# Optimization experiments

Hardware: AMD Instinct MI355X
Metric: run time of the kernel (lower is better)

## Reference

```python
import jax, jax.numpy as jnp
import numpy as np

B = 1 << 21          # shading points per batch
U_RES, CH = 400, 8   # spatial plane
A_RES, ACH = 50, 50 and 8  # placeholder, real consts below
A_RES, ACH = 50, 8   # angular planes (h/d)
HID = 32
IN_CH = CH + 2 * ACH  # 24


def _bilerp_clamp(tex, uv):
    # Bilinear interp, both axes clamped (U-plane). tex: (H,W,C), uv: (B,2) in [0,1]
    H, W, _ = tex.shape
    u = jnp.clip(uv[:, 0], 0.0, 1.0) * (W - 1)
    v = jnp.clip(uv[:, 1], 0.0, 1.0) * (H - 1)
    x0 = jnp.floor(u).astype(jnp.int32)
    x1 = jnp.clip(x0 + 1, 0, W - 1)
    y0 = jnp.floor(v).astype(jnp.int32)
    y1 = jnp.clip(y0 + 1, 0, H - 1)
    ur = (u - x0.astype(u.dtype))[:, None]
    vr = (v - y0.astype(v.dtype))[:, None]
    p00 = tex[y0, x0]; p10 = tex[y0, x1]; p01 = tex[y1, x0]; p11 = tex[y1, x1]
    return ((1 - ur) * (1 - vr) * p00 + ur * (1 - vr) * p10
            + (1 - ur) * vr * p01 + ur * vr * p11)


def _bilerp_wrap_u(tex, uv):
    # Bilinear interp wrapping the u (phi) axis, clamping v (H/D planes).
    H, W, _ = tex.shape
    u = (uv[:, 0] % 1.0) * W
    v = jnp.clip(uv[:, 1], 0.0, 1.0) * (H - 1)
    x0f = jnp.floor(u)
    x0 = x0f.astype(jnp.int32) % W
    x1 = (x0 + 1) % W
    y0 = jnp.floor(v).astype(jnp.int32)
    y1 = jnp.clip(y0 + 1, 0, H - 1)
    ur = (u - x0f)[:, None]
    vr = (v - y0.astype(v.dtype))[:, None]
    p00 = tex[y0, x0]; p10 = tex[y0, x1]; p01 = tex[y1, x0]; p11 = tex[y1, x1]
    return ((1 - ur) * (1 - vr) * p00 + ur * (1 - vr) * p10
            + (1 - ur) * vr * p01 + ur * vr * p11)


def setup_inputs() -> dict:
    key = jax.random.key(0)
    ks = jax.random.split(key, 8)
    x = jax.random.uniform(ks[0], (B, 6), dtype=jnp.float32)
    u_plane = 0.01 * jax.random.normal(ks[1], (U_RES, U_RES, CH), dtype=jnp.float32)
    h_plane = 0.01 * jax.random.normal(ks[2], (A_RES, A_RES, ACH), dtype=jnp.float32)
    d_plane = 0.01 * jax.random.normal(ks[3], (A_RES, A_RES, ACH), dtype=jnp.float32)
    def lin_w(k, fout, fin):  # torch nn.Linear default init (kaiming-uniform-ish)
        lim = 1.0 / np.sqrt(fin)
        return jax.random.uniform(k, (fout, fin), jnp.float32, -lim, lim)
    W0 = lin_w(ks[4], HID, IN_CH)
    W1 = lin_w(ks[5], HID, HID)
    W2 = lin_w(ks[6], HID, HID)
    W3 = lin_w(ks[7], 3, HID)
    return {"x": x, "u_plane": u_plane, "h_plane": h_plane, "d_plane": d_plane,
            "W0": W0, "W1": W1, "W2": W2, "W3": W3}


def reference(x, u_plane, h_plane, d_plane, W0, W1, W2, W3):
    # Split and reorder: H/D planes receive (u=phi, v=theta)
    uv = x[:, 0:2]
    h_uv = jnp.stack((x[:, 3], x[:, 2]), axis=1)
    d_uv = jnp.stack((x[:, 5], x[:, 4]), axis=1)
    fU = _bilerp_clamp(u_plane, uv)       # (B, CH)
    fH = _bilerp_wrap_u(h_plane, h_uv)    # (B, ACH)
    fD = _bilerp_wrap_u(d_plane, d_uv)    # (B, ACH)
    feat = jnp.concatenate([fU, fH, fD], axis=1)  # (B, 24)
    # Quant mode 'off' -> QLinear is a plain bias-free matmul with W^T
    h = jax.nn.relu(feat @ W0.T)
    h = jax.nn.relu(h @ W1.T)
    h = jax.nn.relu(h @ W2.T)
    return h @ W3.T  # (B, 3)
```

## Files before the change

kernel.cpp:

```cpp
#include <hip/hip_runtime.h>

typedef _Float16 half4 __attribute__((ext_vector_type(4)));
typedef _Float16 half8 __attribute__((ext_vector_type(8)));
typedef float floatx4 __attribute__((ext_vector_type(4)));

#define U_RESV 400
#define A_RESV 50

#define UHALVES (U_RESV * U_RESV * 8)
#define AHALVES (A_RESV * A_RESV * 8)
#define WOFF    (UHALVES + 2 * AHALVES)
#define W0OFF   0
#define W1OFF   896
#define W2OFF   2048
#define W3OFF   3200
#define WTOT    3776

__device__ __forceinline__ float clamp01(float x) { return fminf(fmaxf(x, 0.0f), 1.0f); }

__device__ __forceinline__ floatx4 mfma16(half4 a, half4 b, floatx4 c) {
    return __builtin_amdgcn_mfma_f32_16x16x16f16(a, b, c, 0, 0, 0);
}
__device__ __forceinline__ half4 zero4() {
    half4 h; h[0] = h[1] = h[2] = h[3] = (_Float16)0.f; return h;
}
__device__ __forceinline__ half4 relu4(half4 v) {
#if __has_builtin(__builtin_elementwise_max)
    return __builtin_elementwise_max(v, zero4());
#else
    half4 r;
#pragma unroll
    for (int i = 0; i < 4; ++i) r[i] = v[i] > (_Float16)0.f ? v[i] : (_Float16)0.f;
    return r;
#endif
}

__device__ __forceinline__ void cvt_chunk(const float* __restrict__ src,
                                          _Float16* __restrict__ dst, int i) {
    float4 a = *(const float4*)(src + (size_t)i * 8);
    float4 b = *(const float4*)(src + (size_t)i * 8 + 4);
    half8 h;
    h[0] = (_Float16)a.x; h[1] = (_Float16)a.y; h[2] = (_Float16)a.z; h[3] = (_Float16)a.w;
    h[4] = (_Float16)b.x; h[5] = (_Float16)b.y; h[6] = (_Float16)b.z; h[7] = (_Float16)b.w;
    *(half8*)(dst + (size_t)i * 8) = h;
}

__device__ __forceinline__ void wblob_fill(const float* __restrict__ W0,
                                           const float* __restrict__ W1,
                                           const float* __restrict__ W2,
                                           const float* __restrict__ W3,
                                           _Float16* __restrict__ w, int tid, int nthr) {
    for (int i = tid; i < WTOT; i += nthr) {
        float v;
        if (i < W1OFF) {
            int r = i / 28, c = i - r * 28;
            v = (c < 24) ? W0[r * 24 + c] : 0.f;
        } else if (i < W2OFF) {
            int j = i - W1OFF, r = j / 36, c = j - r * 36;
            v = (c < 32) ? W1[r * 32 + c] : 0.f;
        } else if (i < W3OFF) {
            int j = i - W2OFF, r = j / 36, c = j - r * 36;
            v = (c < 32) ? W2[r * 32 + c] : 0.f;
        } else {
            int j = i - W3OFF, r = j / 36, c = j - r * 36;
            v = (r < 3 && c < 32) ? W3[r * 32 + c] : 0.f;
        }
        w[i] = (_Float16)v;
    }
}

__global__ __launch_bounds__(256) void pconv_kernel(
    const float* __restrict__ u_plane, const float* __restrict__ h_plane,
    const float* __restrict__ d_plane, const float* __restrict__ W0,
    const float* __restrict__ W1, const float* __restrict__ W2,
    const float* __restrict__ W3, _Float16* __restrict__ dst) {
    const int gid = blockIdx.x * 256 + threadIdx.x;
    const int gsz = gridDim.x * 256;
    for (int i = gid; i < UHALVES / 8; i += gsz) cvt_chunk(u_plane, dst, i);
    for (int i = gid; i < AHALVES / 8; i += gsz) cvt_chunk(h_plane, dst + UHALVES, i);
    for (int i = gid; i < AHALVES / 8; i += gsz) cvt_chunk(d_plane, dst + UHALVES + AHALVES, i);
    if (blockIdx.x == 0) wblob_fill(W0, W1, W2, W3, dst + WOFF, threadIdx.x, 256);
}

__global__ __launch_bounds__(256) void wprep_kernel(
    const float* __restrict__ W0, const float* __restrict__ W1,
    const float* __restrict__ W2, const float* __restrict__ W3,
    _Float16* __restrict__ wdst) {
    wblob_fill(W0, W1, W2, W3, wdst, threadIdx.x, 256);
}

struct GA { int o0, o1, o2, o3; float w00, w10, w01, w11; };

__device__ __forceinline__ GA mkU(float ux, float uy) {
    GA g;
    float u = clamp01(ux) * (float)(U_RESV - 1);
    float v = clamp01(uy) * (float)(U_RESV - 1);
    float x0f = floorf(u), y0f = floorf(v);
    int x0 = (int)x0f, y0 = (int)y0f;
    int x1 = min(x0 + 1, U_RESV - 1), y1 = min(y0 + 1, U_RESV - 1);
    float ur = u - x0f, vr = v - y0f;
    g.w00 = (1.0f - ur) * (1.0f - vr); g.w10 = ur * (1.0f - vr);
    g.w01 = (1.0f - ur) * vr;          g.w11 = ur * vr;
    g.o0 = (y0 * U_RESV + x0) * 8;
    g.o1 = (y0 * U_RESV + x1) * 8;
    g.o2 = (y1 * U_RESV + x0) * 8;
    g.o3 = (y1 * U_RESV + x1) * 8;
    return g;
}
__device__ __forceinline__ GA mkA(float uu, float vv) {
    GA g;
    float uf = uu - floorf(uu);
    float u = uf * (float)A_RESV;
    float v = clamp01(vv) * (float)(A_RESV - 1);
    float x0f = floorf(u), y0f = floorf(v);
    int x0 = (int)x0f;
    int x1 = x0 + 1; if (x1 == A_RESV) x1 = 0;
    int y0 = (int)y0f;
    int y1 = min(y0 + 1, A_RESV - 1);
    float ur = u - x0f, vr = v - y0f;
    g.w00 = (1.0f - ur) * (1.0f - vr); g.w10 = ur * (1.0f - vr);
    g.w01 = (1.0f - ur) * vr;          g.w11 = ur * vr;
    g.o0 = (y0 * A_RESV + x0) * 8;
    g.o1 = (y0 * A_RESV + x1) * 8;
    g.o2 = (y1 * A_RESV + x0) * 8;
    g.o3 = (y1 * A_RESV + x1) * 8;
    return g;
}

__device__ __forceinline__ void blend8(half8 a, half8 b, half8 c, half8 d,
                                       const GA& g, float* f) {
#pragma unroll
    for (int i = 0; i < 8; ++i) {
        float r = (float)a[i] * g.w00;
        r = fmaf((float)b[i], g.w10, r);
        r = fmaf((float)c[i], g.w01, r);
        r = fmaf((float)d[i], g.w11, r);
        f[i] = r;
    }
}


template <int K>
__global__ __launch_bounds__(256, 2) void tpmlp_pipe(
    const float* __restrict__ x,
    const _Float16* __restrict__ up,
    const _Float16* __restrict__ hp,
    const _Float16* __restrict__ dp,
    const _Float16* __restrict__ wsw,
    float* __restrict__ out) {
    const int tid  = threadIdx.x;
    const int lane = tid & 63;
    const int wv   = tid >> 6;
    const int q    = lane >> 4;
    const int c15  = lane & 15;

    __shared__ __align__(16) _Float16 fl[256 * 28];
    __shared__ __align__(16) _Float16 wl[WTOT];

    {
        const uint4* src = (const uint4*)wsw;
        uint4 a = src[tid];
        uint4 b;
        if (tid < 472 - 256) b = src[256 + tid];
        uint4* dst = (uint4*)wl;
        dst[tid] = a;
        if (tid < 472 - 256) dst[256 + tid] = b;
    }
    __syncthreads();

    const _Float16* wb  = fl + (size_t)wv * 64 * 28;
    const _Float16* w0l = wl + W0OFF;
    const _Float16* w1l = wl + W1OFF;
    const _Float16* w2l = wl + W2OFF;
    const _Float16* w3l = wl + W3OFF;
    const size_t blkbase = (size_t)blockIdx.x * (256 * K);

    auto xload = [&](int it, float2& a, float2& b, float2& c) {
        const float2* p = (const float2*)(x + (blkbase + (size_t)it * 256 + tid) * 6);
        a = p[0]; b = p[1]; c = p[2];
    };

    float2 c01, c23, c45;
    float2 n01, n23, n45;
    xload(0, c01, c23, c45);
    if (K > 1) xload(1, n01, n23, n45);

    GA gU = mkU(c01.x, c01.y);
    GA gH = mkA(c23.y, c23.x);
    GA gD = mkA(c45.y, c45.x);
    half8 tU0 = *(const half8*)(up + gU.o0);
    half8 tU1 = *(const half8*)(up + gU.o1);
    half8 tU2 = *(const half8*)(up + gU.o2);
    half8 tU3 = *(const half8*)(up + gU.o3);
    half8 tH0 = *(const half8*)(hp + gH.o0);
    half8 tH1 = *(const half8*)(hp + gH.o1);
    half8 tH2 = *(const half8*)(hp + gH.o2);
    half8 tH3 = *(const half8*)(hp + gH.o3);
    half8 tD0 = *(const half8*)(dp + gD.o0);
    half8 tD1 = *(const half8*)(dp + gD.o1);
    half8 tD2 = *(const half8*)(dp + gD.o2);
    half8 tD3 = *(const half8*)(dp + gD.o3);
    __builtin_amdgcn_sched_barrier(0);

#pragma unroll
    for (int it = 0; it < K; ++it) {
        GA pU, pH, pD;
        half8 mU0, mU1, mU2, mU3, mH0, mH1, mH2, mH3, mD0, mD1, mD2, mD3;
        float2 f01 = n01, f23 = n23, f45 = n45;
        if (it + 2 < K) xload(it + 2, n01, n23, n45);
        if (it + 1 < K) {
            pU = mkU(f01.x, f01.y);
            pH = mkA(f23.y, f23.x);
            pD = mkA(f45.y, f45.x);
            mU0 = *(const half8*)(up + pU.o0);
            mU1 = *(const half8*)(up + pU.o1);
            mU2 = *(const half8*)(up + pU.o2);
            mU3 = *(const half8*)(up + pU.o3);
            mH0 = *(const half8*)(hp + pH.o0);
            mH1 = *(const half8*)(hp + pH.o1);
            mH2 = *(const half8*)(hp + pH.o2);
            mH3 = *(const half8*)(hp + pH.o3);
            mD0 = *(const half8*)(dp + pD.o0);
            mD1 = *(const half8*)(dp + pD.o1);
            mD2 = *(const half8*)(dp + pD.o2);
            mD3 = *(const half8*)(dp + pD.o3);
            __builtin_amdgcn_sched_barrier(0);
        }

        float fU[8], fH[8], fD[8];
        blend8(tU0, tU1, tU2, tU3, gU, fU);
        blend8(tH0, tH1, tH2, tH3, gH, fH);
        blend8(tD0, tD1, tD2, tD3, gD, fD);

        {
            _Float16* row = fl + tid * 28;
            half8 hU, hH, hD;
#pragma unroll
            for (int i = 0; i < 8; ++i) {
                hU[i] = (_Float16)fU[i];
                hH[i] = (_Float16)fH[i];
                hD[i] = (_Float16)fD[i];
            }
            *(half8*)(row)      = hU;
            *(half8*)(row + 8)  = hH;
            *(half8*)(row + 16) = hD;
        }
        asm volatile("s_waitcnt lgkmcnt(0)" ::: "memory");
        __builtin_amdgcn_sched_barrier(0);

        floatx4 zf; zf[0] = 0.f; zf[1] = 0.f; zf[2] = 0.f; zf[3] = 0.f;
        half4 b0[4], b1[4];
#pragma unroll
        for (int j = 0; j < 4; ++j) {
            const _Float16* r = wb + (size_t)(j * 16 + c15) * 28;
            b0[j] = *(const half4*)(r + q * 4);
            b1[j] = (q < 2) ? *(const half4*)(r + 16 + q * 4) : zero4();
        }

        floatx4 cc[2][4];
#pragma unroll
        for (int m = 0; m < 2; ++m) {
            half4 a0 = *(const half4*)(w0l + (size_t)(16 * m + c15) * 28 + q * 4);
            half4 a1 = (q < 2) ? *(const half4*)(w0l + (size_t)(16 * m + c15) * 28 + 16 + q * 4) : zero4();
#pragma unroll
            for (int j = 0; j < 4; ++j)
                cc[m][j] = mfma16(a1, b1[j], mfma16(a0, b0[j], zf));
        }
#pragma unroll
        for (int j = 0; j < 4; ++j) {
#pragma unroll
            for (int e = 0; e < 4; ++e) {
                b0[j][e] = (_Float16)cc[0][j][e];
                b1[j][e] = (_Float16)cc[1][j][e];
            }
            b0[j] = relu4(b0[j]);
            b1[j] = relu4(b1[j]);
        }

#pragma unroll
        for (int m = 0; m < 2; ++m) {
            half4 a0 = *(const half4*)(w1l + (size_t)(16 * m + c15) * 36 + q * 4);
            half4 a1 = *(const half4*)(w1l + (size_t)(16 * m + c15) * 36 + 16 + q * 4);
#pragma unroll
            for (int j = 0; j < 4; ++j)
                cc[m][j] = mfma16(a1, b1[j], mfma16(a0, b0[j], zf));
        }
#pragma unroll
        for (int j = 0; j < 4; ++j) {
#pragma unroll
            for (int e = 0; e < 4; ++e) {
                b0[j][e] = (_Float16)cc[0][j][e];
                b1[j][e] = (_Float16)cc[1][j][e];
            }
            b0[j] = relu4(b0[j]);
            b1[j] = relu4(b1[j]);
        }

#pragma unroll
        for (int m = 0; m < 2; ++m) {
            half4 a0 = *(const half4*)(w2l + (size_t)(16 * m + c15) * 36 + q * 4);
            half4 a1 = *(const half4*)(w2l + (size_t)(16 * m + c15) * 36 + 16 + q * 4);
#pragma unroll
            for (int j = 0; j < 4; ++j)
                cc[m][j] = mfma16(a1, b1[j], mfma16(a0, b0[j], zf));
        }
#pragma unroll
        for (int j = 0; j < 4; ++j) {
#pragma unroll
            for (int e = 0; e < 4; ++e) {
                b0[j][e] = (_Float16)cc[0][j][e];
                b1[j][e] = (_Float16)cc[1][j][e];
            }
            b0[j] = relu4(b0[j]);
            b1[j] = relu4(b1[j]);
        }

        floatx4 c3[4];
        {
            half4 a0 = *(const half4*)(w3l + (size_t)c15 * 36 + q * 4);
            half4 a1 = *(const half4*)(w3l + (size_t)c15 * 36 + 16 + q * 4);
#pragma unroll
            for (int j = 0; j < 4; ++j)
                c3[j] = mfma16(a1, b1[j], mfma16(a0, b0[j], zf));
        }

        if (lane < 16) {
            const size_t base = blkbase + (size_t)it * 256 + (size_t)wv * 64;
#pragma unroll
            for (int j = 0; j < 4; ++j) {
                size_t p = base + (size_t)j * 16 + lane;
                float* o = out + p * 3;
                o[0] = c3[j][0];
                o[1] = c3[j][1];
                o[2] = c3[j][2];
            }
        }

        if (it + 1 < K) {
            gU = pU; gH = pH; gD = pD;
            tU0 = mU0; tU1 = mU1; tU2 = mU2; tU3 = mU3;
            tH0 = mH0; tH1 = mH1; tH2 = mH2; tH3 = mH3;
            tD0 = mD0; tD1 = mD1; tD2 = mD2; tD3 = mD3;
        }
    }
}

__global__ __launch_bounds__(512, 2) void tpmlp_f32(
    const float* __restrict__ x,
    const float* __restrict__ up,
    const float* __restrict__ hp,
    const float* __restrict__ dp,
    const _Float16* __restrict__ wsw,
    float* __restrict__ out) {
    const int tid  = threadIdx.x;
    const int lane = tid & 63;
    const int wv   = tid >> 6;
    const int q    = lane >> 4;
    const int c15  = lane & 15;

    __shared__ __align__(16) _Float16 fl[512 * 28];
    __shared__ __align__(16) _Float16 wl[WTOT];

    const size_t P = (size_t)blockIdx.x * 512 + tid;
    const float2* xp = (const float2*)(x + P * 6);
    float2 p01v = xp[0], p23v = xp[1], p45v = xp[2];

    uint4 w_a;
    if (tid < 472) w_a = ((const uint4*)wsw)[tid];

    GA gU = mkU(p01v.x, p01v.y);
    GA gH = mkA(p23v.y, p23v.x);
    GA gD = mkA(p45v.y, p45v.x);

    float4 sU0 = *(const float4*)(up + gU.o0); float4 rU0 = *(const float4*)(up + gU.o0 + 4);
    float4 sU1 = *(const float4*)(up + gU.o1); float4 rU1 = *(const float4*)(up + gU.o1 + 4);
    float4 sU2 = *(const float4*)(up + gU.o2); float4 rU2 = *(const float4*)(up + gU.o2 + 4);
    float4 sU3 = *(const float4*)(up + gU.o3); float4 rU3 = *(const float4*)(up + gU.o3 + 4);
    float4 sH0 = *(const float4*)(hp + gH.o0); float4 rH0 = *(const float4*)(hp + gH.o0 + 4);
    float4 sH1 = *(const float4*)(hp + gH.o1); float4 rH1 = *(const float4*)(hp + gH.o1 + 4);
    float4 sH2 = *(const float4*)(hp + gH.o2); float4 rH2 = *(const float4*)(hp + gH.o2 + 4);
    float4 sH3 = *(const float4*)(hp + gH.o3); float4 rH3 = *(const float4*)(hp + gH.o3 + 4);
    float4 sD0 = *(const float4*)(dp + gD.o0); float4 rD0 = *(const float4*)(dp + gD.o0 + 4);
    float4 sD1 = *(const float4*)(dp + gD.o1); float4 rD1 = *(const float4*)(dp + gD.o1 + 4);
    float4 sD2 = *(const float4*)(dp + gD.o2); float4 rD2 = *(const float4*)(dp + gD.o2 + 4);
    float4 sD3 = *(const float4*)(dp + gD.o3); float4 rD3 = *(const float4*)(dp + gD.o3 + 4);
    __builtin_amdgcn_sched_barrier(0);

    if (tid < 472) ((uint4*)wl)[tid] = w_a;
    asm volatile("s_waitcnt lgkmcnt(0)" ::: "memory");
    __builtin_amdgcn_s_barrier();

    float fU[8], fH[8], fD[8];
#pragma unroll
    for (int i = 0; i < 8; ++i) {
        const float* a = i < 4 ? (const float*)&sU0 : (const float*)&rU0;
        const float* b = i < 4 ? (const float*)&sU1 : (const float*)&rU1;
        const float* c = i < 4 ? (const float*)&sU2 : (const float*)&rU2;
        const float* d = i < 4 ? (const float*)&sU3 : (const float*)&rU3;
        int k = i & 3;
        float r = a[k] * gU.w00;
        r = fmaf(b[k], gU.w10, r);
        r = fmaf(c[k], gU.w01, r);
        r = fmaf(d[k], gU.w11, r);
        fU[i] = r;
    }
#pragma unroll
    for (int i = 0; i < 8; ++i) {
        const float* a = i < 4 ? (const float*)&sH0 : (const float*)&rH0;
        const float* b = i < 4 ? (const float*)&sH1 : (const float*)&rH1;
        const float* c = i < 4 ? (const float*)&sH2 : (const float*)&rH2;
        const float* d = i < 4 ? (const float*)&sH3 : (const float*)&rH3;
        int k = i & 3;
        float r = a[k] * gH.w00;
        r = fmaf(b[k], gH.w10, r);
        r = fmaf(c[k], gH.w01, r);
        r = fmaf(d[k], gH.w11, r);
        fH[i] = r;
    }
#pragma unroll
    for (int i = 0; i < 8; ++i) {
        const float* a = i < 4 ? (const float*)&sD0 : (const float*)&rD0;
        const float* b = i < 4 ? (const float*)&sD1 : (const float*)&rD1;
        const float* c = i < 4 ? (const float*)&sD2 : (const float*)&rD2;
        const float* d = i < 4 ? (const float*)&sD3 : (const float*)&rD3;
        int k = i & 3;
        float r = a[k] * gD.w00;
        r = fmaf(b[k], gD.w10, r);
        r = fmaf(c[k], gD.w01, r);
        r = fmaf(d[k], gD.w11, r);
        fD[i] = r;
    }

    {
        _Float16* row = fl + tid * 28;
        half8 hU, hH, hD;
#pragma unroll
        for (int i = 0; i < 8; ++i) {
            hU[i] = (_Float16)fU[i];
            hH[i] = (_Float16)fH[i];
            hD[i] = (_Float16)fD[i];
        }
        *(half8*)(row)      = hU;
        *(half8*)(row + 8)  = hH;
        *(half8*)(row + 16) = hD;
    }
    asm volatile("s_waitcnt lgkmcnt(0)" ::: "memory");
    __builtin_amdgcn_sched_barrier(0);

    floatx4 zf; zf[0] = 0.f; zf[1] = 0.f; zf[2] = 0.f; zf[3] = 0.f;
    const _Float16* wb = fl + (size_t)wv * 64 * 28;
    const _Float16* w0l = wl + W0OFF;
    const _Float16* w1l = wl + W1OFF;
    const _Float16* w2l = wl + W2OFF;
    const _Float16* w3l = wl + W3OFF;

    half4 b0[4], b1[4];
#pragma unroll
    for (int j = 0; j < 4; ++j) {
        const _Float16* r = wb + (size_t)(j * 16 + c15) * 28;
        b0[j] = *(const half4*)(r + q * 4);
        b1[j] = (q < 2) ? *(const half4*)(r + 16 + q * 4) : zero4();
    }

    floatx4 cc[2][4];
#pragma unroll
    for (int m = 0; m < 2; ++m) {
        half4 a0 = *(const half4*)(w0l + (size_t)(16 * m + c15) * 28 + q * 4);
        half4 a1 = (q < 2) ? *(const half4*)(w0l + (size_t)(16 * m + c15) * 28 + 16 + q * 4) : zero4();
#pragma unroll
        for (int j = 0; j < 4; ++j)
            cc[m][j] = mfma16(a1, b1[j], mfma16(a0, b0[j], zf));
    }
#pragma unroll
    for (int j = 0; j < 4; ++j) {
#pragma unroll
        for (int e = 0; e < 4; ++e) {
            b0[j][e] = (_Float16)cc[0][j][e];
            b1[j][e] = (_Float16)cc[1][j][e];
        }
        b0[j] = relu4(b0[j]);
        b1[j] = relu4(b1[j]);
    }
#pragma unroll
    for (int m = 0; m < 2; ++m) {
        half4 a0 = *(const half4*)(w1l + (size_t)(16 * m + c15) * 36 + q * 4);
        half4 a1 = *(const half4*)(w1l + (size_t)(16 * m + c15) * 36 + 16 + q * 4);
#pragma unroll
        for (int j = 0; j < 4; ++j)
            cc[m][j] = mfma16(a1, b1[j], mfma16(a0, b0[j], zf));
    }
#pragma unroll
    for (int j = 0; j < 4; ++j) {
#pragma unroll
        for (int e = 0; e < 4; ++e) {
            b0[j][e] = (_Float16)cc[0][j][e];
            b1[j][e] = (_Float16)cc[1][j][e];
        }
        b0[j] = relu4(b0[j]);
        b1[j] = relu4(b1[j]);
    }
#pragma unroll
    for (int m = 0; m < 2; ++m) {
        half4 a0 = *(const half4*)(w2l + (size_t)(16 * m + c15) * 36 + q * 4);
        half4 a1 = *(const half4*)(w2l + (size_t)(16 * m + c15) * 36 + 16 + q * 4);
#pragma unroll
        for (int j = 0; j < 4; ++j)
            cc[m][j] = mfma16(a1, b1[j], mfma16(a0, b0[j], zf));
    }
#pragma unroll
    for (int j = 0; j < 4; ++j) {
#pragma unroll
        for (int e = 0; e < 4; ++e) {
            b0[j][e] = (_Float16)cc[0][j][e];
            b1[j][e] = (_Float16)cc[1][j][e];
        }
        b0[j] = relu4(b0[j]);
        b1[j] = relu4(b1[j]);
    }

    floatx4 c3[4];
    {
        half4 a0 = *(const half4*)(w3l + (size_t)c15 * 36 + q * 4);
        half4 a1 = *(const half4*)(w3l + (size_t)c15 * 36 + 16 + q * 4);
#pragma unroll
        for (int j = 0; j < 4; ++j)
            c3[j] = mfma16(a1, b1[j], mfma16(a0, b0[j], zf));
    }

    if (lane < 16) {
        const size_t base = (size_t)blockIdx.x * 512 + (size_t)wv * 64;
#pragma unroll
        for (int j = 0; j < 4; ++j) {
            size_t p = base + (size_t)j * 16 + lane;
            float* o = out + p * 3;
            o[0] = c3[j][0];
            o[1] = c3[j][1];
            o[2] = c3[j][2];
        }
    }
}

extern "C" void kernel_launch(void* const* d_in, const int* in_sizes, int n_in,
                              void* d_out, int out_size, void* d_ws, size_t ws_size,
                              hipStream_t stream) {
    const float* x       = (const float*)d_in[0];
    const float* u_plane = (const float*)d_in[1];
    const float* h_plane = (const float*)d_in[2];
    const float* d_plane = (const float*)d_in[3];
    const float* W0      = (const float*)d_in[4];
    const float* W1      = (const float*)d_in[5];
    const float* W2      = (const float*)d_in[6];
    const float* W3      = (const float*)d_in[7];
    float* out = (float*)d_out;
    _Float16* wsw = (_Float16*)d_ws;

    int n = in_sizes[0] / 6;
    constexpr int K = 8;

    const size_t need = ((size_t)WOFF + WTOT) * 2;
    if (ws_size >= need) {
        pconv_kernel<<<648, 256, 0, stream>>>(u_plane, h_plane, d_plane,
                                              W0, W1, W2, W3, wsw);
        int grid = n / (256 * K);
        tpmlp_pipe<K><<<grid, 256, 0, stream>>>(
            x, wsw, wsw + UHALVES, wsw + UHALVES + AHALVES, wsw + WOFF, out);
    } else {
        wprep_kernel<<<1, 256, 0, stream>>>(W0, W1, W2, W3, wsw);
        tpmlp_f32<<<n / 512, 512, 0, stream>>>(
            x, u_plane, h_plane, d_plane, wsw, out);
    }
}
```

Baseline: 75.52 us.

## Stage angular planes in LDS, use 1024-thread blocks, drop software prefetch

The fp16 H and D angular planes are copied into shared memory once per block, so their gathers become LDS reads instead of global or L2 loads. Blocks grow from 256 to 1024 threads with K reduced to 2, and the explicit register double-buffered prefetch of x and texel gathers is removed in favour of a simple non-unrolled loop that relies on occupancy to hide latency. This adds about 80KB of LDS per block (features, angular planes, weights), which limits how many blocks fit per CU. It also adds a per-block LDS fill and possible bank conflicts on random gathers.

```diff
diff --git a/kernel.cpp b/kernel.cpp
--- a/kernel.cpp
+++ b/kernel.cpp
@@ -141,11 +141,10 @@
 
 
 template <int K>
-__global__ __launch_bounds__(256, 2) void tpmlp_pipe(
+__global__ __launch_bounds__(1024, 4) void tpmlp_kernel(
     const float* __restrict__ x,
     const _Float16* __restrict__ up,
-    const _Float16* __restrict__ hp,
-    const _Float16* __restrict__ dp,
+    const _Float16* __restrict__ hdsrc,
     const _Float16* __restrict__ wsw,
     float* __restrict__ out) {
     const int tid  = threadIdx.x;
@@ -154,83 +153,57 @@
     const int q    = lane >> 4;
     const int c15  = lane & 15;
 
-    __shared__ __align__(16) _Float16 fl[256 * 28];
+    __shared__ __align__(16) _Float16 fl[1024 * 28];
+    __shared__ __align__(16) _Float16 hdl[2 * AHALVES];
     __shared__ __align__(16) _Float16 wl[WTOT];
 
     {
-        const uint4* src = (const uint4*)wsw;
-        uint4 a = src[tid];
-        uint4 b;
-        if (tid < 472 - 256) b = src[256 + tid];
-        uint4* dst = (uint4*)wl;
-        dst[tid] = a;
-        if (tid < 472 - 256) dst[256 + tid] = b;
+        const uint4* src = (const uint4*)hdsrc;
+        uint4* dst = (uint4*)hdl;
+        for (int i = tid; i < (2 * AHALVES) / 8; i += 1024) dst[i] = src[i];
+        if (tid < 472) ((uint4*)wl)[tid] = ((const uint4*)wsw)[tid];
     }
     __syncthreads();
 
+    const _Float16* hp  = hdl;
+    const _Float16* dp  = hdl + AHALVES;
     const _Float16* wb  = fl + (size_t)wv * 64 * 28;
     const _Float16* w0l = wl + W0OFF;
     const _Float16* w1l = wl + W1OFF;
     const _Float16* w2l = wl + W2OFF;
     const _Float16* w3l = wl + W3OFF;
-    const size_t blkbase = (size_t)blockIdx.x * (256 * K);
-
-    auto xload = [&](int it, float2& a, float2& b, float2& c) {
-        const float2* p = (const float2*)(x + (blkbase + (size_t)it * 256 + tid) * 6);
-        a = p[0]; b = p[1]; c = p[2];
-    };
-
-    float2 c01, c23, c45;
-    float2 n01, n23, n45;
-    xload(0, c01, c23, c45);
-    if (K > 1) xload(1, n01, n23, n45);
-
-    GA gU = mkU(c01.x, c01.y);
-    GA gH = mkA(c23.y, c23.x);
-    GA gD = mkA(c45.y, c45.x);
-    half8 tU0 = *(const half8*)(up + gU.o0);
-    half8 tU1 = *(const half8*)(up + gU.o1);
-    half8 tU2 = *(const half8*)(up + gU.o2);
-    half8 tU3 = *(const half8*)(up + gU.o3);
-    half8 tH0 = *(const half8*)(hp + gH.o0);
-    half8 tH1 = *(const half8*)(hp + gH.o1);
-    half8 tH2 = *(const half8*)(hp + gH.o2);
-    half8 tH3 = *(const half8*)(hp + gH.o3);
-    half8 tD0 = *(const half8*)(dp + gD.o0);
-    half8 tD1 = *(const half8*)(dp + gD.o1);
-    half8 tD2 = *(const half8*)(dp + gD.o2);
-    half8 tD3 = *(const half8*)(dp + gD.o3);
-    __builtin_amdgcn_sched_barrier(0);
-
-#pragma unroll
+    const size_t blkbase = (size_t)blockIdx.x * (1024 * K);
+
+#pragma unroll 1
     for (int it = 0; it < K; ++it) {
-        GA pU, pH, pD;
-        half8 mU0, mU1, mU2, mU3, mH0, mH1, mH2, mH3, mD0, mD1, mD2, mD3;
-        float2 f01 = n01, f23 = n23, f45 = n45;
-        if (it + 2 < K) xload(it + 2, n01, n23, n45);
-        if (it + 1 < K) {
-            pU = mkU(f01.x, f01.y);
-            pH = mkA(f23.y, f23.x);
-            pD = mkA(f45.y, f45.x);
-            mU0 = *(const half8*)(up + pU.o0);
-            mU1 = *(const half8*)(up + pU.o1);
-            mU2 = *(const half8*)(up + pU.o2);
-            mU3 = *(const half8*)(up + pU.o3);
-            mH0 = *(const half8*)(hp + pH.o0);
-            mH1 = *(const half8*)(hp + pH.o1);
-            mH2 = *(const half8*)(hp + pH.o2);
-            mH3 = *(const half8*)(hp + pH.o3);
-            mD0 = *(const half8*)(dp + pD.o0);
-            mD1 = *(const half8*)(dp + pD.o1);
-            mD2 = *(const half8*)(dp + pD.o2);
-            mD3 = *(const half8*)(dp + pD.o3);
-            __builtin_amdgcn_sched_barrier(0);
-        }
+        const size_t P = blkbase + (size_t)it * 1024 + tid;
+
+        const float2* xp = (const float2*)(x + P * 6);
+        float2 p01v = xp[0], p23v = xp[1], p45v = xp[2];
+
+        GA gU = mkU(p01v.x, p01v.y);
+        GA gH = mkA(p23v.y, p23v.x);
+        GA gD = mkA(p45v.y, p45v.x);
+
+        half8 tU0 = *(const half8*)(up + gU.o0);
+        half8 tU1 = *(const half8*)(up + gU.o1);
+        half8 tU2 = *(const half8*)(up + gU.o2);
+        half8 tU3 = *(const half8*)(up + gU.o3);
+        __builtin_amdgcn_sched_barrier(0);
+
+        half8 tH0 = *(const half8*)(hp + gH.o0);
+        half8 tH1 = *(const half8*)(hp + gH.o1);
+        half8 tH2 = *(const half8*)(hp + gH.o2);
+        half8 tH3 = *(const half8*)(hp + gH.o3);
+        half8 tD0 = *(const half8*)(dp + gD.o0);
+        half8 tD1 = *(const half8*)(dp + gD.o1);
+        half8 tD2 = *(const half8*)(dp + gD.o2);
+        half8 tD3 = *(const half8*)(dp + gD.o3);
 
         float fU[8], fH[8], fD[8];
-        blend8(tU0, tU1, tU2, tU3, gU, fU);
         blend8(tH0, tH1, tH2, tH3, gH, fH);
         blend8(tD0, tD1, tD2, tD3, gD, fD);
+        blend8(tU0, tU1, tU2, tU3, gU, fU);
 
         {
             _Float16* row = fl + tid * 28;
@@ -325,7 +298,7 @@
         }
 
         if (lane < 16) {
-            const size_t base = blkbase + (size_t)it * 256 + (size_t)wv * 64;
+            const size_t base = blkbase + (size_t)it * 1024 + (size_t)wv * 64;
 #pragma unroll
             for (int j = 0; j < 4; ++j) {
                 size_t p = base + (size_t)j * 16 + lane;
@@ -334,13 +307,6 @@
                 o[1] = c3[j][1];
                 o[2] = c3[j][2];
             }
-        }
-
-        if (it + 1 < K) {
-            gU = pU; gH = pH; gD = pD;
-            tU0 = mU0; tU1 = mU1; tU2 = mU2; tU3 = mU3;
-            tH0 = mH0; tH1 = mH1; tH2 = mH2; tH3 = mH3;
-            tD0 = mD0; tD1 = mD1; tD2 = mD2; tD3 = mD3;
         }
     }
 }
@@ -555,15 +521,15 @@
     _Float16* wsw = (_Float16*)d_ws;
 
     int n = in_sizes[0] / 6;
-    constexpr int K = 8;
+    constexpr int K = 2;
 
     const size_t need = ((size_t)WOFF + WTOT) * 2;
     if (ws_size >= need) {
         pconv_kernel<<<648, 256, 0, stream>>>(u_plane, h_plane, d_plane,
                                               W0, W1, W2, W3, wsw);
-        int grid = n / (256 * K);
-        tpmlp_pipe<K><<<grid, 256, 0, stream>>>(
-            x, wsw, wsw + UHALVES, wsw + UHALVES + AHALVES, wsw + WOFF, out);
+        int grid = n / (1024 * K);
+        tpmlp_kernel<K><<<grid, 1024, 0, stream>>>(
+            x, wsw, wsw + UHALVES, wsw + WOFF, out);
     } else {
         wprep_kernel<<<1, 256, 0, stream>>>(W0, W1, W2, W3, wsw);
         tpmlp_f32<<<n / 512, 512, 0, stream>>>(
```

Measured after the change: 67.01 us. 11.3% less time.
